# Performance work log

Hardware: AMD Instinct MI355X
Metric: run time of the kernel (lower is better)

Reference implementation:

```python
import jax, jax.numpy as jnp
import numpy as np

NUM_USERS = 100000
NUM_ITEMS = 50000
N_NODES = NUM_USERS + NUM_ITEMS
EMB = 64          # emb_dim == layers[0]
NNZ = 2_400_000   # ~16 avg degree normalized-Laplacian nonzeros
BATCH = 16384


def spmm(rows, cols, vals, x, n):
    # sparse (COO) Laplacian @ dense features: out[r] += v * x[c]
    return jax.ops.segment_sum(vals[:, None] * x[cols], rows, num_segments=n)


def setup_inputs() -> dict:
    key = jax.random.key(0)
    ks = jax.random.split(key, 20)
    userIdx = jax.random.randint(ks[0], (BATCH,), 0, NUM_USERS)
    itemIdx = jax.random.randint(ks[1], (BATCH,), 0, NUM_ITEMS)
    lap_rows = jax.random.randint(ks[2], (NNZ,), 0, N_NODES, dtype=jnp.int32)
    lap_cols = jax.random.randint(ks[3], (NNZ,), 0, N_NODES, dtype=jnp.int32)
    # normalized Laplacian values ~ 1/sqrt(deg_i*deg_j), small positive
    lap_vals = jax.random.uniform(ks[4], (NNZ,), dtype=jnp.float32) * 0.05
    uEmb = jax.random.normal(ks[5], (NUM_USERS, EMB), dtype=jnp.float32) * 0.1
    iEmb = jax.random.normal(ks[6], (NUM_ITEMS, EMB), dtype=jnp.float32) * 0.1
    s = 1.0 / np.sqrt(EMB)
    gW0 = jax.random.normal(ks[7], (EMB, EMB), dtype=jnp.float32) * s
    gb0 = jnp.zeros((EMB,), jnp.float32)
    gW1 = jax.random.normal(ks[8], (EMB, EMB), dtype=jnp.float32) * s
    gb1 = jnp.zeros((EMB,), jnp.float32)
    D_CAT = EMB * 3 * 2  # 384
    W1 = jax.random.normal(ks[9], (D_CAT, 64), dtype=jnp.float32) / np.sqrt(D_CAT)
    b1 = jnp.zeros((64,), jnp.float32)
    W2 = jax.random.normal(ks[10], (64, 32), dtype=jnp.float32) / 8.0
    b2 = jnp.zeros((32,), jnp.float32)
    W3 = jax.random.normal(ks[11], (32, 1), dtype=jnp.float32) / np.sqrt(32.0)
    b3 = jnp.zeros((1,), jnp.float32)
    return {"userIdx": userIdx, "itemIdx": itemIdx,
            "lap_rows": lap_rows, "lap_cols": lap_cols, "lap_vals": lap_vals,
            "uEmb": uEmb, "iEmb": iEmb,
            "gW0": gW0, "gb0": gb0, "gW1": gW1, "gb1": gb1,
            "W1": W1, "b1": b1, "W2": W2, "b2": b2, "W3": W3, "b3": b3}


def reference(userIdx, itemIdx, lap_rows, lap_cols, lap_vals,
              uEmb, iEmb, gW0, gb0, gW1, gb1, W1, b1, W2, b2, W3, b3):
    features = jnp.concatenate([uEmb, iEmb], axis=0)  # [N, EMB]
    final = features
    for W, b in ((gW0, gb0), (gW1, gb1)):
        # (Laplacian + selfLoop I) @ features, then linear + ReLU
        h = spmm(lap_rows, lap_cols, lap_vals, features, N_NODES) + features
        features = jax.nn.relu(h @ W + b)
        final = jnp.concatenate([final, features], axis=1)
    u = final[userIdx]                     # [B, 192]
    it = final[itemIdx + NUM_USERS]        # [B, 192]
    e = jnp.concatenate([u, it], axis=1)   # [B, 384]
    e = jax.nn.relu(e @ W1 + b1)
    e = e @ W2 + b2
    e = e @ W3 + b3
    return e.ravel()
```

## Files before the change

kernel.cpp:

```cpp
#include <hip/hip_runtime.h>
#include <hip/hip_bf16.h>

#define NUM_USERS 100000
#define NUM_ITEMS 50000
#define N_NODES   150000
#define EMB       64
#define NNZ       2400000
#define BATCH     16384
#define D_CAT     384
#define BSHIFT    8
#define NBUCK     ((N_NODES + 255) >> 8)
#define EPB       8192

__device__ __forceinline__ unsigned short f2bf(float f) {
    unsigned u = __float_as_uint(f);
    unsigned r = u + 0x7fffu + ((u >> 16) & 1u);
    return (unsigned short)(r >> 16);
}
__device__ __forceinline__ float bflo(unsigned u) { return __uint_as_float(u << 16); }
__device__ __forceinline__ float bfhi(unsigned u) { return __uint_as_float(u & 0xffff0000u); }

__global__ __launch_bounds__(1024) void bucket_hist(const int* __restrict__ rows,
                                                    int* __restrict__ bcnt, int nnz) {
    __shared__ int h[NBUCK];
    int tid = threadIdx.x;
    for (int i = tid; i < NBUCK; i += 1024) h[i] = 0;
    __syncthreads();
    for (int i = blockIdx.x * 1024 + tid; i < nnz; i += gridDim.x * 1024)
        atomicAdd(&h[rows[i] >> BSHIFT], 1);
    __syncthreads();
    for (int i = tid; i < NBUCK; i += 1024) {
        int c = h[i];
        if (c) atomicAdd(&bcnt[i], c);
    }
}

__global__ __launch_bounds__(1024) void bucket_scan(const int* __restrict__ bcnt,
                                                    int* __restrict__ boffs,
                                                    int* __restrict__ gtails, int nnz) {
    __shared__ int s[1024];
    int t = threadIdx.x;
    int x = (t < NBUCK) ? bcnt[t] : 0;
    s[t] = x;
    __syncthreads();
#pragma unroll
    for (int off = 1; off < 1024; off <<= 1) {
        int v = (t >= off) ? s[t - off] : 0;
        __syncthreads();
        s[t] += v;
        __syncthreads();
    }
    if (t < NBUCK) {
        int e = s[t] - x;
        boffs[t] = e;
        gtails[t] = e;
    }
    if (t == 0) boffs[NBUCK] = nnz;
}

__global__ __launch_bounds__(1024) void coarse_multisplit(const int* __restrict__ rows,
                                                          const int* __restrict__ cols,
                                                          const float* __restrict__ vals,
                                                          int* __restrict__ gtails,
                                                          int2* __restrict__ pv, int nnz) {
    __shared__ int hcnt[NBUCK];
    int tid = threadIdx.x;
    int e0 = blockIdx.x * EPB;
    int e1 = e0 + EPB < nnz ? e0 + EPB : nnz;

    for (int i = tid; i < NBUCK; i += 1024) hcnt[i] = 0;
    __syncthreads();
    for (int i = e0 + tid; i < e1; i += 1024)
        atomicAdd(&hcnt[rows[i] >> BSHIFT], 1);
    __syncthreads();
    for (int i = tid; i < NBUCK; i += 1024) {
        int c = hcnt[i];
        if (c) hcnt[i] = atomicAdd(&gtails[i], c);
    }
    __syncthreads();
    for (int i = e0 + tid; i < e1; i += 1024) {
        int r = rows[i];
        int pos = atomicAdd(&hcnt[r >> BSHIFT], 1);
        pv[pos] = make_int2(((r & 255) << 18) | cols[i], __float_as_int(vals[i]));
    }
}

__global__ __launch_bounds__(1024) void fine_scatter(const int* __restrict__ boffs,
                                                     const int2* __restrict__ pv,
                                                     int2* __restrict__ packed,
                                                     int* __restrict__ row_ptr, int nnz) {
    __shared__ int rcnt[256];
    __shared__ int loff[256];
    int b = blockIdx.x;
    int tid = threadIdx.x;
    int lo = boffs[b], hi = boffs[b + 1];
    int r0 = b << BSHIFT;
    int nr = N_NODES - r0; if (nr > 256) nr = 256;

    if (tid < 256) rcnt[tid] = 0;
    __syncthreads();
    for (int i = lo + tid; i < hi; i += 1024)
        atomicAdd(&rcnt[pv[i].x >> 18], 1);
    __syncthreads();
    if (tid < 256) loff[tid] = rcnt[tid];
    __syncthreads();
#pragma unroll
    for (int off = 1; off < 256; off <<= 1) {
        int v = (tid < 256 && tid >= off) ? loff[tid - off] : 0;
        __syncthreads();
        if (tid < 256) loff[tid] += v;
        __syncthreads();
    }
    if (tid < 256) {
        int e = lo + loff[tid] - rcnt[tid];
        loff[tid] = e;
        if (tid < nr) row_ptr[r0 + tid] = e;
    }
    if (b == 0 && tid == 0) row_ptr[N_NODES] = nnz;
    __syncthreads();
    for (int i = lo + tid; i < hi; i += 1024) {
        int2 e = pv[i];
        int rl = e.x >> 18;
        int pos = atomicAdd(&loff[rl], 1);
        packed[pos] = make_int2(e.x & 0x3FFFF, e.y);
    }
}

__global__ __launch_bounds__(256) void gemm_table_f32(const float* __restrict__ uE,
                                                      const float* __restrict__ iE,
                                                      const float* __restrict__ W,
                                                      unsigned short* __restrict__ Zh,
                                                      int n_rows) {
    __shared__ float Wl[64 * 64];
    __shared__ float Xf[64 * 64];
    int tid = threadIdx.x;
    int lane = tid & 63;
    int wave = tid >> 6;
    int r0 = blockIdx.x * 64;
    int last = n_rows - 1;

    for (int i = tid; i < 64 * 64; i += 256) Wl[i] = W[i];
    for (int i = tid; i < 64 * 16; i += 256) {
        int row = i >> 4, q = i & 15;
        int r = r0 + row; r = r > last ? last : r;
        const float4* src = (r < NUM_USERS)
            ? (const float4*)(uE + (size_t)r * 64)
            : (const float4*)(iE + (size_t)(r - NUM_USERS) * 64);
        ((float4*)Xf)[i] = src[q];
    }
    __syncthreads();

    int rbase = wave * 16;
    float acc[16];
#pragma unroll
    for (int i = 0; i < 16; ++i) acc[i] = 0.f;

#pragma unroll 1
    for (int kc = 0; kc < 16; ++kc) {
        float w0 = Wl[(kc * 4 + 0) * 64 + lane];
        float w1 = Wl[(kc * 4 + 1) * 64 + lane];
        float w2 = Wl[(kc * 4 + 2) * 64 + lane];
        float w3 = Wl[(kc * 4 + 3) * 64 + lane];
#pragma unroll
        for (int i = 0; i < 16; ++i) {
            float4 q = ((const float4*)Xf)[(rbase + i) * 16 + kc];
            acc[i] = fmaf(q.x, w0, acc[i]);
            acc[i] = fmaf(q.y, w1, acc[i]);
            acc[i] = fmaf(q.z, w2, acc[i]);
            acc[i] = fmaf(q.w, w3, acc[i]);
        }
    }
#pragma unroll
    for (int i = 0; i < 16; ++i) {
        int r = r0 + rbase + i;
        if (r < n_rows) Zh[(size_t)r * 64 + lane] = f2bf(acc[i]);
    }
}

__global__ __launch_bounds__(256) void gemm_table_bf16(const unsigned* __restrict__ Xh,
                                                       const float* __restrict__ W,
                                                       unsigned short* __restrict__ Zh,
                                                       int n_rows) {
    __shared__ float Wl[64 * 64];
    __shared__ uint4 Xl4[64 * 8];
    int tid = threadIdx.x;
    int lane = tid & 63;
    int wave = tid >> 6;
    int r0 = blockIdx.x * 64;
    int nr = n_rows - r0; if (nr > 64) nr = 64;

    for (int i = tid; i < 64 * 64; i += 256) Wl[i] = W[i];
    const uint4* Xg4 = (const uint4*)(Xh + (size_t)r0 * 32);
    for (int i = tid; i < nr * 8; i += 256) Xl4[i] = Xg4[i];
    __syncthreads();

    const unsigned* Xl = (const unsigned*)Xl4;
    int rbase = wave * 16;
    float acc[16];
#pragma unroll
    for (int i = 0; i < 16; ++i) acc[i] = 0.f;

#pragma unroll 1
    for (int kc = 0; kc < 8; ++kc) {
        float w0 = Wl[(kc * 8 + 0) * 64 + lane];
        float w1 = Wl[(kc * 8 + 1) * 64 + lane];
        float w2 = Wl[(kc * 8 + 2) * 64 + lane];
        float w3 = Wl[(kc * 8 + 3) * 64 + lane];
        float w4 = Wl[(kc * 8 + 4) * 64 + lane];
        float w5 = Wl[(kc * 8 + 5) * 64 + lane];
        float w6 = Wl[(kc * 8 + 6) * 64 + lane];
        float w7 = Wl[(kc * 8 + 7) * 64 + lane];
#pragma unroll
        for (int i = 0; i < 16; ++i) {
            uint4 q = *(const uint4*)&Xl[(rbase + i) * 32 + kc * 4];
            acc[i] = fmaf(bflo(q.x), w0, acc[i]);
            acc[i] = fmaf(bfhi(q.x), w1, acc[i]);
            acc[i] = fmaf(bflo(q.y), w2, acc[i]);
            acc[i] = fmaf(bfhi(q.y), w3, acc[i]);
            acc[i] = fmaf(bflo(q.z), w4, acc[i]);
            acc[i] = fmaf(bfhi(q.z), w5, acc[i]);
            acc[i] = fmaf(bflo(q.w), w6, acc[i]);
            acc[i] = fmaf(bfhi(q.w), w7, acc[i]);
        }
    }
#pragma unroll
    for (int i = 0; i < 16; ++i) {
        int r = r0 + rbase + i;
        if (r < n_rows) Zh[(size_t)r * 64 + lane] = f2bf(acc[i]);
    }
}

__global__ __launch_bounds__(256) void spmm_bias_relu(const int* __restrict__ row_ptr,
                                                      const int2* __restrict__ packed,
                                                      const uint2* __restrict__ zh2,
                                                      const float* __restrict__ bias,
                                                      uint2* __restrict__ outh2,
                                                      int n_rows) {
    int tid = threadIdx.x;
    int lane = tid & 63;
    int wave = tid >> 6;
    int q = lane >> 4;
    int k = lane & 15;
    int r = blockIdx.x * 4 + wave;
    if (r >= n_rows) return;

    uint2 su = zh2[(size_t)r * 16 + k];
    float4 acc;
    acc.x = q ? 0.f : bflo(su.x);
    acc.y = q ? 0.f : bfhi(su.x);
    acc.z = q ? 0.f : bflo(su.y);
    acc.w = q ? 0.f : bfhi(su.y);

    int e = row_ptr[r] + q;
    int end = row_ptr[r + 1];
    for (; e + 13 < end; e += 16) {
        int2 p0 = packed[e + 0];
        int2 p1 = packed[e + 4];
        int2 p2 = packed[e + 8];
        int2 p3 = packed[e + 12];
        uint2 z0 = zh2[(size_t)p0.x * 16 + k];
        uint2 z1 = zh2[(size_t)p1.x * 16 + k];
        uint2 z2 = zh2[(size_t)p2.x * 16 + k];
        uint2 z3 = zh2[(size_t)p3.x * 16 + k];
        float v0 = __int_as_float(p0.y), v1 = __int_as_float(p1.y);
        float v2 = __int_as_float(p2.y), v3 = __int_as_float(p3.y);
        acc.x = fmaf(v0, bflo(z0.x), acc.x); acc.y = fmaf(v0, bfhi(z0.x), acc.y);
        acc.z = fmaf(v0, bflo(z0.y), acc.z); acc.w = fmaf(v0, bfhi(z0.y), acc.w);
        acc.x = fmaf(v1, bflo(z1.x), acc.x); acc.y = fmaf(v1, bfhi(z1.x), acc.y);
        acc.z = fmaf(v1, bflo(z1.y), acc.z); acc.w = fmaf(v1, bfhi(z1.y), acc.w);
        acc.x = fmaf(v2, bflo(z2.x), acc.x); acc.y = fmaf(v2, bfhi(z2.x), acc.y);
        acc.z = fmaf(v2, bflo(z2.y), acc.z); acc.w = fmaf(v2, bfhi(z2.y), acc.w);
        acc.x = fmaf(v3, bflo(z3.x), acc.x); acc.y = fmaf(v3, bfhi(z3.x), acc.y);
        acc.z = fmaf(v3, bflo(z3.y), acc.z); acc.w = fmaf(v3, bfhi(z3.y), acc.w);
    }
    for (; e < end; e += 4) {
        int2 p = packed[e];
        uint2 z = zh2[(size_t)p.x * 16 + k];
        float v = __int_as_float(p.y);
        acc.x = fmaf(v, bflo(z.x), acc.x); acc.y = fmaf(v, bfhi(z.x), acc.y);
        acc.z = fmaf(v, bflo(z.y), acc.z); acc.w = fmaf(v, bfhi(z.y), acc.w);
    }

    acc.x += __shfl_xor(acc.x, 16, 64);
    acc.y += __shfl_xor(acc.y, 16, 64);
    acc.z += __shfl_xor(acc.z, 16, 64);
    acc.w += __shfl_xor(acc.w, 16, 64);
    acc.x += __shfl_xor(acc.x, 32, 64);
    acc.y += __shfl_xor(acc.y, 32, 64);
    acc.z += __shfl_xor(acc.z, 32, 64);
    acc.w += __shfl_xor(acc.w, 32, 64);
    if (q == 0) {
        float4 bv = ((const float4*)bias)[k];
        float a = fmaxf(acc.x + bv.x, 0.f);
        float b = fmaxf(acc.y + bv.y, 0.f);
        float c = fmaxf(acc.z + bv.z, 0.f);
        float d = fmaxf(acc.w + bv.w, 0.f);
        outh2[(size_t)r * 16 + k] = make_uint2(
            ((unsigned)f2bf(b) << 16) | (unsigned)f2bf(a),
            ((unsigned)f2bf(d) << 16) | (unsigned)f2bf(c));
    }
}

__global__ __launch_bounds__(256) void fused_mlp(
        const int* __restrict__ userIdx, const int* __restrict__ itemIdx,
        const float* __restrict__ uEmb, const float* __restrict__ iEmb,
        const unsigned short* __restrict__ feat1h,
        const unsigned short* __restrict__ feat2h,
        const float* __restrict__ W1, const float* __restrict__ b1,
        const float* __restrict__ W2, const float* __restrict__ b2,
        const float* __restrict__ W3, const float* __restrict__ b3,
        float* __restrict__ out) {
    __shared__ float    Wl[128 * 64];
    __shared__ unsigned El[64 * 64];
    __shared__ float    Ht[64 * 64];
    __shared__ float    W2l[64 * 32];
    __shared__ float    w3l[32];
    __shared__ float    b2l[32];
    __shared__ int      uidx[64], iidx[64];
    int tid = threadIdx.x;
    int lane = tid & 63;
    int wave = tid >> 6;
    int r0 = blockIdx.x * 64;
    int rbase = wave * 16;

    if (tid < 64) uidx[tid] = userIdx[r0 + tid];
    else if (tid < 128) iidx[tid - 64] = itemIdx[r0 + tid - 64];
    if (tid < 32) { w3l[tid] = W3[tid]; b2l[tid] = b2[tid]; }
    for (int i = tid; i < 64 * 32; i += 256) W2l[i] = W2[i];

    float acc[16];
    float bv = b1[lane];
#pragma unroll
    for (int i = 0; i < 16; ++i) acc[i] = bv;

#pragma unroll 1
    for (int c = 0; c < 3; ++c) {
        __syncthreads();
        for (int i = tid; i < 128 * 64; i += 256) Wl[i] = W1[c * 128 * 64 + i];
        for (int t = tid; t < 1024; t += 256) {
            int row = t >> 4;
            int seg = (t >> 3) & 1;
            int q   = t & 7;
            int gseg = c * 2 + seg;
            uint4 val;
            if (gseg == 0 || gseg == 3) {
                const float* p = (gseg == 0)
                    ? uEmb + (size_t)uidx[row] * 64 + q * 8
                    : iEmb + (size_t)iidx[row] * 64 + q * 8;
                float4 a = *(const float4*)p;
                float4 b = *(const float4*)(p + 4);
                val.x = ((unsigned)f2bf(a.y) << 16) | f2bf(a.x);
                val.y = ((unsigned)f2bf(a.w) << 16) | f2bf(a.z);
                val.z = ((unsigned)f2bf(b.y) << 16) | f2bf(b.x);
                val.w = ((unsigned)f2bf(b.w) << 16) | f2bf(b.z);
            } else {
                const unsigned short* src;
                if (gseg == 1)      src = feat1h + (size_t)uidx[row] * 64;
                else if (gseg == 2) src = feat2h + (size_t)uidx[row] * 64;
                else if (gseg == 4) src = feat1h + (size_t)(iidx[row] + NUM_USERS) * 64;
                else                src = feat2h + (size_t)(iidx[row] + NUM_USERS) * 64;
                val = *(const uint4*)(src + q * 8);
            }
            *(uint4*)&El[row * 64 + seg * 32 + q * 4] = val;
        }
        __syncthreads();
        const uint4* El4 = (const uint4*)El;
#pragma unroll 1
        for (int k = 0; k < 128; k += 8) {
            float w0 = Wl[(k + 0) * 64 + lane];
            float w1 = Wl[(k + 1) * 64 + lane];
            float w2 = Wl[(k + 2) * 64 + lane];
            float w3 = Wl[(k + 3) * 64 + lane];
            float w4 = Wl[(k + 4) * 64 + lane];
            float w5 = Wl[(k + 5) * 64 + lane];
            float w6 = Wl[(k + 6) * 64 + lane];
            float w7 = Wl[(k + 7) * 64 + lane];
#pragma unroll
            for (int i = 0; i < 16; ++i) {
                uint4 q = El4[(rbase + i) * 16 + (k >> 3)];
                acc[i] = fmaf(bflo(q.x), w0, acc[i]);
                acc[i] = fmaf(bfhi(q.x), w1, acc[i]);
                acc[i] = fmaf(bflo(q.y), w2, acc[i]);
                acc[i] = fmaf(bfhi(q.y), w3, acc[i]);
                acc[i] = fmaf(bflo(q.z), w4, acc[i]);
                acc[i] = fmaf(bfhi(q.z), w5, acc[i]);
                acc[i] = fmaf(bflo(q.w), w6, acc[i]);
                acc[i] = fmaf(bfhi(q.w), w7, acc[i]);
            }
        }
    }

#pragma unroll
    for (int i = 0; i < 16; ++i) Ht[(rbase + i) * 64 + lane] = fmaxf(acc[i], 0.f);
    __syncthreads();

    int half = lane >> 5;
    int k = lane & 31;
    float b3v = b3[0];
#pragma unroll 1
    for (int p = 0; p < 8; ++p) {
        int row = rbase + p * 2 + half;
        float z = b2l[k];
#pragma unroll
        for (int j = 0; j < 64; ++j)
            z = fmaf(Ht[row * 64 + j], W2l[j * 32 + k], z);
        z *= w3l[k];
#pragma unroll
        for (int off = 16; off; off >>= 1)
            z += __shfl_xor(z, off, 64);
        if (k == 0) out[r0 + row] = z + b3v;
    }
}

extern "C" void kernel_launch(void* const* d_in, const int* in_sizes, int n_in,
                              void* d_out, int out_size, void* d_ws, size_t ws_size,
                              hipStream_t stream) {
    const int*   userIdx = (const int*)  d_in[0];
    const int*   itemIdx = (const int*)  d_in[1];
    const int*   lap_rows= (const int*)  d_in[2];
    const int*   lap_cols= (const int*)  d_in[3];
    const float* lap_vals= (const float*)d_in[4];
    const float* uEmb    = (const float*)d_in[5];
    const float* iEmb    = (const float*)d_in[6];
    const float* gW0     = (const float*)d_in[7];
    const float* gb0     = (const float*)d_in[8];
    const float* gW1     = (const float*)d_in[9];
    const float* gb1     = (const float*)d_in[10];
    const float* W1      = (const float*)d_in[11];
    const float* b1      = (const float*)d_in[12];
    const float* W2      = (const float*)d_in[13];
    const float* b2      = (const float*)d_in[14];
    const float* W3      = (const float*)d_in[15];
    const float* b3      = (const float*)d_in[16];
    float* out = (float*)d_out;

    const size_t NF = (size_t)N_NODES * EMB;
    char* w = (char*)d_ws;
    unsigned short* bufA = (unsigned short*)w;
    unsigned short* bufB = bufA + NF;
    char*  region3 = (char*)(bufB + NF);
    int2*  pv      = (int2*)region3;
    unsigned short* Zh = (unsigned short*)region3;
    int2*  packed  = (int2*)(region3 + NF * sizeof(float));
    int*   row_ptr = (int*)(packed + NNZ);
    int*   boffs   = row_ptr + (N_NODES + 1);
    int*   gtails  = boffs + (NBUCK + 1);
    int*   bcnt    = gtails + NBUCK;

    const int ms_grid   = (NNZ + EPB - 1) / EPB;
    const int spmm_grid = (N_NODES + 3) / 4;
    const int gemm_grid = (N_NODES + 63) / 64;

    hipMemsetAsync(bcnt, 0, NBUCK * sizeof(int), stream);
    bucket_hist<<<128, 1024, 0, stream>>>(lap_rows, bcnt, NNZ);
    bucket_scan<<<1, 1024, 0, stream>>>(bcnt, boffs, gtails, NNZ);
    coarse_multisplit<<<ms_grid, 1024, 0, stream>>>(lap_rows, lap_cols, lap_vals,
                                                    gtails, pv, NNZ);
    fine_scatter<<<NBUCK, 1024, 0, stream>>>(boffs, pv, packed, row_ptr, NNZ);

    gemm_table_f32<<<gemm_grid, 256, 0, stream>>>(uEmb, iEmb, gW0, Zh, N_NODES);
    spmm_bias_relu<<<spmm_grid, 256, 0, stream>>>(row_ptr, packed, (const uint2*)Zh,
                                                  gb0, (uint2*)bufA, N_NODES);

    gemm_table_bf16<<<gemm_grid, 256, 0, stream>>>((const unsigned*)bufA, gW1, Zh, N_NODES);
    spmm_bias_relu<<<spmm_grid, 256, 0, stream>>>(row_ptr, packed, (const uint2*)Zh,
                                                  gb1, (uint2*)bufB, N_NODES);

    fused_mlp<<<BATCH / 64, 256, 0, stream>>>(userIdx, itemIdx, uEmb, iEmb,
                                              bufA, bufB, W1, b1, W2, b2, W3, b3, out);
}
```

Baseline: 496.8 us.

## Stage coarse multisplit in LDS for coalesced bucket-contiguous global writes

The coarse multisplit kernel now first scatters each block's elements into a locally bucket-sorted shared-memory staging buffer. A per-element offset map then lets threads write the staged pairs to global memory in contiguous runs per bucket, replacing the previous random 8-byte scatter writes. The elements-per-block count is raised to 9375, giving exactly 256 blocks. The cost is about 112 KB of dynamic LDS per block, which limits occupancy to one block per CU, plus an extra block-wide scan and a serial per-bucket fill loop.

```diff
diff --git a/kernel.cpp b/kernel.cpp
--- a/kernel.cpp
+++ b/kernel.cpp
@@ -10,7 +10,7 @@
 #define D_CAT     384
 #define BSHIFT    8
 #define NBUCK     ((N_NODES + 255) >> 8)
-#define EPB       8192
+#define EPB       9375
 
 __device__ __forceinline__ unsigned short f2bf(float f) {
     unsigned u = __float_as_uint(f);
@@ -63,26 +63,60 @@
                                                           const float* __restrict__ vals,
                                                           int* __restrict__ gtails,
                                                           int2* __restrict__ pv, int nnz) {
+    extern __shared__ int dyn[];
+    int2* stage = (int2*)dyn;
+    int*  smap  = dyn + 2 * EPB;
     __shared__ int hcnt[NBUCK];
+    __shared__ int lstart[NBUCK];
+    __shared__ int shiftv[NBUCK];
+
     int tid = threadIdx.x;
     int e0 = blockIdx.x * EPB;
     int e1 = e0 + EPB < nnz ? e0 + EPB : nnz;
+    int nE = e1 - e0;
 
     for (int i = tid; i < NBUCK; i += 1024) hcnt[i] = 0;
     __syncthreads();
     for (int i = e0 + tid; i < e1; i += 1024)
         atomicAdd(&hcnt[rows[i] >> BSHIFT], 1);
     __syncthreads();
-    for (int i = tid; i < NBUCK; i += 1024) {
-        int c = hcnt[i];
-        if (c) hcnt[i] = atomicAdd(&gtails[i], c);
-    }
-    __syncthreads();
+
+    int cnt = (tid < NBUCK) ? hcnt[tid] : 0;
+    smap[tid] = cnt;
+    __syncthreads();
+#pragma unroll
+    for (int off = 1; off < 1024; off <<= 1) {
+        int v = (tid >= off) ? smap[tid - off] : 0;
+        __syncthreads();
+        smap[tid] += v;
+        __syncthreads();
+    }
+    if (tid < NBUCK) {
+        int ls = smap[tid] - cnt;
+        lstart[tid] = ls;
+        hcnt[tid] = ls;
+        int gb = cnt ? atomicAdd(&gtails[tid], cnt) : 0;
+        shiftv[tid] = gb - ls;
+    }
+    __syncthreads();
+
+    for (int b = tid; b < NBUCK; b += 1024) {
+        int beg = lstart[b];
+        int end_ = (b == NBUCK - 1) ? nE : lstart[b + 1];
+        int sh = shiftv[b];
+        for (int k = beg; k < end_; ++k) smap[k] = sh;
+    }
+    __syncthreads();
+
     for (int i = e0 + tid; i < e1; i += 1024) {
         int r = rows[i];
-        int pos = atomicAdd(&hcnt[r >> BSHIFT], 1);
-        pv[pos] = make_int2(((r & 255) << 18) | cols[i], __float_as_int(vals[i]));
-    }
+        int p = atomicAdd(&hcnt[r >> BSHIFT], 1);
+        stage[p] = make_int2(((r & 255) << 18) | cols[i], __float_as_int(vals[i]));
+    }
+    __syncthreads();
+
+    for (int j = tid; j < nE; j += 1024)
+        pv[smap[j] + j] = stage[j];
 }
 
 __global__ __launch_bounds__(1024) void fine_scatter(const int* __restrict__ boffs,
@@ -448,14 +482,15 @@
     int*   bcnt    = gtails + NBUCK;
 
     const int ms_grid   = (NNZ + EPB - 1) / EPB;
+    const int ms_lds    = EPB * 12;
     const int spmm_grid = (N_NODES + 3) / 4;
     const int gemm_grid = (N_NODES + 63) / 64;
 
     hipMemsetAsync(bcnt, 0, NBUCK * sizeof(int), stream);
     bucket_hist<<<128, 1024, 0, stream>>>(lap_rows, bcnt, NNZ);
     bucket_scan<<<1, 1024, 0, stream>>>(bcnt, boffs, gtails, NNZ);
-    coarse_multisplit<<<ms_grid, 1024, 0, stream>>>(lap_rows, lap_cols, lap_vals,
-                                                    gtails, pv, NNZ);
+    coarse_multisplit<<<ms_grid, 1024, ms_lds, stream>>>(lap_rows, lap_cols, lap_vals,
+                                                         gtails, pv, NNZ);
     fine_scatter<<<NBUCK, 1024, 0, stream>>>(boffs, pv, packed, row_ptr, NNZ);
 
     gemm_table_f32<<<gemm_grid, 256, 0, stream>>>(uEmb, iEmb, gW0, Zh, N_NODES);
```

Measured after the change: 471.9 us. -5.0%, faster.
